# Performance work log

Hardware: AMD Instinct MI355X
Metric: run time of the kernel (lower is better)

The kernel has to match this reference:

```python
import jax, jax.numpy as jnp
import numpy as np

B, DIM, H, W = 8, 256, 128, 128
P = 4               # patch_size
HEADS = 8
HD = DIM // HEADS   # head dim = 32
CPB_HIDDEN = 512    # hidden width of the dynamic RPE MLP


def setup_inputs() -> dict:
    key = jax.random.key(0)
    ks = jax.random.split(key, 12)
    s = 0.02
    return {
        "x": jax.random.normal(ks[0], (B, DIM, H, W), dtype=jnp.float32),
        # PatchEmbed2d: Conv2d(dim, dim, kernel=P, stride=P)  weight [O, I, P, P]
        "w_embed": jax.random.normal(ks[1], (DIM, DIM, P, P), dtype=jnp.float32) * s,
        "b_embed": jnp.zeros((DIM,), dtype=jnp.float32),
        # DynamicPosEncoder: MLP(2 -> CPB_HIDDEN -> HEADS) on relative coords
        "cpb_w1": jax.random.normal(ks[2], (CPB_HIDDEN, 2), dtype=jnp.float32) * s,
        "cpb_b1": jnp.zeros((CPB_HIDDEN,), dtype=jnp.float32),
        "cpb_w2": jax.random.normal(ks[3], (HEADS, CPB_HIDDEN), dtype=jnp.float32) * s,
        # MaskAttention2d
        "w_qkv": jax.random.normal(ks[4], (3 * DIM, DIM), dtype=jnp.float32) * s,
        "b_qkv": jnp.zeros((3 * DIM,), dtype=jnp.float32),
        "w_proj": jax.random.normal(ks[5], (DIM, DIM), dtype=jnp.float32) * s,
        "b_proj": jnp.zeros((DIM,), dtype=jnp.float32),
        # PatchUnEmbed2d: ConvTranspose2d(dim, dim, kernel=P, stride=P)  weight [I, O, P, P]
        "w_unembed": jax.random.normal(ks[6], (DIM, DIM, P, P), dtype=jnp.float32) * s,
        "b_unembed": jnp.zeros((DIM,), dtype=jnp.float32),
    }


def _rpe_bias(Hp, Wp, cpb_w1, cpb_b1, cpb_w2):
    """Dynamic relative position bias -> [HEADS, N, N], N = Hp*Wp."""
    # continuous relative-coordinate table [(2Hp-1)*(2Wp-1), 2], normalized to [-1, 1]
    rh = (jnp.arange(2 * Hp - 1, dtype=jnp.float32) - (Hp - 1)) / max(Hp - 1, 1)
    rw = (jnp.arange(2 * Wp - 1, dtype=jnp.float32) - (Wp - 1)) / max(Wp - 1, 1)
    rel = jnp.stack(jnp.meshgrid(rh, rw, indexing="ij"), axis=-1).reshape(-1, 2)
    table = jax.nn.relu(rel @ cpb_w1.T + cpb_b1) @ cpb_w2.T  # [(2Hp-1)(2Wp-1), HEADS]
    # static relative position index [N, N]
    ch = np.arange(Hp)
    cw = np.arange(Wp)
    coords = np.stack(np.meshgrid(ch, cw, indexing="ij")).reshape(2, -1)  # [2, N]
    d = coords[:, :, None] - coords[:, None, :]                           # [2, N, N]
    idx = (d[0] + Hp - 1) * (2 * Wp - 1) + (d[1] + Wp - 1)               # [N, N]
    bias = table[jnp.asarray(idx)]                                        # [N, N, HEADS]
    return bias.transpose(2, 0, 1)                                        # [HEADS, N, N]


def reference(x, w_embed, b_embed, cpb_w1, cpb_b1, cpb_w2,
              w_qkv, b_qkv, w_proj, b_proj, w_unembed, b_unembed):
    Bx, C, Hf, Wf = x.shape
    Hp, Wp = Hf // P, Wf // P
    N = Hp * Wp
    # ---- patch embed: Conv2d(k=P, s=P) as block reshape + einsum ----
    xr = x.reshape(Bx, C, Hp, P, Wp, P)
    z = jnp.einsum("bchpwq,ocpq->bohw", xr, w_embed) + b_embed[None, :, None, None]
    # ---- dynamic RPE bias ----
    bias = _rpe_bias(Hp, Wp, cpb_w1, cpb_b1, cpb_w2)  # [HEADS, N, N]
    # ---- multi-head self-attention over the Hp*Wp grid ----
    tok = z.reshape(Bx, C, N).transpose(0, 2, 1)                     # [B, N, C]
    qkv = tok @ w_qkv.T + b_qkv                                       # [B, N, 3C]
    qkv = qkv.reshape(Bx, N, 3, HEADS, HD).transpose(2, 0, 3, 1, 4)   # [3, B, H, N, hd]
    q, k, v = qkv[0], qkv[1], qkv[2]
    scale = HD ** -0.5
    attn = jnp.einsum("bhnd,bhmd->bhnm", q * scale, k) + bias[None]   # [B, H, N, N]
    attn = jax.nn.softmax(attn, axis=-1)
    out = jnp.einsum("bhnm,bhmd->bhnd", attn, v)                      # [B, H, N, hd]
    out = out.transpose(0, 2, 1, 3).reshape(Bx, N, C)
    out = out @ w_proj.T + b_proj                                     # [B, N, C]
    z2 = out.transpose(0, 2, 1).reshape(Bx, C, Hp, Wp)
    # ---- patch unembed: ConvTranspose2d(k=P, s=P) as einsum + block reshape ----
    y = jnp.einsum("bchw,copq->bohpwq", z2, w_unembed)
    y = y.reshape(Bx, C, Hf, Wf) + b_unembed[None, :, None, None]
    return y
```

## Files before the change

### kernel.cpp

```cpp
#include <hip/hip_runtime.h>
#include <cstdint>
#include <cstddef>


typedef __bf16 bf16x8 __attribute__((ext_vector_type(8)));
typedef float f32x4 __attribute__((ext_vector_type(4)));
typedef unsigned short u16x4 __attribute__((ext_vector_type(4)));

__device__ __forceinline__ unsigned short f2bf(float f) {
  unsigned u = __builtin_bit_cast(unsigned, f);
  u += 0x7fffu + ((u >> 16) & 1u);
  return (unsigned short)(u >> 16);
}
__device__ __forceinline__ float bf2f(unsigned short u) {
  return __builtin_bit_cast(float, ((unsigned)u) << 16);
}

__device__ __forceinline__ void async_ld16(const void* g, void* l) {
  __builtin_amdgcn_global_load_lds(
      (const __attribute__((address_space(1))) void*)g,
      (__attribute__((address_space(3))) void*)l, 16, 0, 0);
}

__global__ __launch_bounds__(256) void rpe_table_kernel(
    const float* __restrict__ w1, const float* __restrict__ b1,
    const float* __restrict__ w2, float* __restrict__ tableT) {
  int t = blockIdx.x * 256 + threadIdx.x;
  if (t >= 3969) return;
  int a = t / 63, c = t - a * 63;
  float rh = (float)(a - 31) * (1.0f / 31.0f);
  float rw = (float)(c - 31) * (1.0f / 31.0f);
  float acc[8];
#pragma unroll
  for (int h = 0; h < 8; h++) acc[h] = 0.f;
  for (int j = 0; j < 512; j++) {
    float hv = fmaxf(rh * w1[2 * j] + rw * w1[2 * j + 1] + b1[j], 0.f);
#pragma unroll
    for (int h = 0; h < 8; h++) acc[h] += hv * w2[h * 512 + j];
  }
#pragma unroll
  for (int h = 0; h < 8; h++) tableT[h * 4096 + t] = acc[h];
}

__global__ __launch_bounds__(256) void cvt_bf16_kernel(
    const float* __restrict__ src, unsigned short* __restrict__ dst, int n8) {
  int i = blockIdx.x * 256 + threadIdx.x;
  if (i >= n8) return;
  const float4* s4 = (const float4*)src + (size_t)i * 2;
  float4 a = s4[0], b = s4[1];
  unsigned short t[8] = {f2bf(a.x), f2bf(a.y), f2bf(a.z), f2bf(a.w),
                         f2bf(b.x), f2bf(b.y), f2bf(b.z), f2bf(b.w)};
  *(uint4*)(dst + (size_t)i * 8) = *(const uint4*)t;
}

__global__ __launch_bounds__(256) void transpose_cvt_kernel(
    const float* __restrict__ src, unsigned short* __restrict__ dst) {
  __shared__ float tile[32][33];
  int bx = blockIdx.x;
  int by = blockIdx.y;
  int tx = threadIdx.x & 31, ty = threadIdx.x >> 5;
#pragma unroll
  for (int r = 0; r < 32; r += 8)
    tile[ty + r][tx] = src[(size_t)(by * 32 + ty + r) * 4096 + bx * 32 + tx];
  __syncthreads();
#pragma unroll
  for (int r = 0; r < 32; r += 8)
    dst[(size_t)(bx * 32 + ty + r) * 256 + by * 32 + tx] = f2bf(tile[tx][ty + r]);
}

__global__ __launch_bounds__(256) void im2col_bf16_kernel(
    const float* __restrict__ x, unsigned short* __restrict__ A) {
  int gid = blockIdx.x * 256 + threadIdx.x;
  int bn = gid & 8191;
  int c = gid >> 13;
  int b = bn >> 10;
  int hw = bn & 1023;
  int h = hw >> 5, w = hw & 31;
  const float4* x4 = (const float4*)x;
  int base = ((b * 256 + c) * 128 + 4 * h) * 32 + w;
  unsigned short t[16];
#pragma unroll
  for (int p = 0; p < 4; p++) {
    float4 v = x4[base + p * 32];
    t[p * 4 + 0] = f2bf(v.x); t[p * 4 + 1] = f2bf(v.y);
    t[p * 4 + 2] = f2bf(v.z); t[p * 4 + 3] = f2bf(v.w);
  }
  unsigned short* dst = A + (size_t)bn * 4096 + c * 16;
  *(uint4*)dst = *(const uint4*)t;
  *(uint4*)(dst + 8) = *(const uint4*)(t + 8);
}

__global__ __launch_bounds__(256) void splitk_reduce_kernel(
    const float* __restrict__ part, const float* __restrict__ bias,
    unsigned short* __restrict__ out) {
  size_t i = ((size_t)blockIdx.x * 256 + threadIdx.x) * 8;
  const float4* p = (const float4*)(part + i);
  const size_t s4 = 2097152 / 4;
  float4 a0 = p[0], a1 = p[1];
#pragma unroll
  for (int s = 1; s < 4; s++) {
    float4 b0 = p[s * s4], b1 = p[s * s4 + 1];
    a0.x += b0.x; a0.y += b0.y; a0.z += b0.z; a0.w += b0.w;
    a1.x += b1.x; a1.y += b1.y; a1.z += b1.z; a1.w += b1.w;
  }
  int col = (int)(i & 255);
  unsigned short t8[8] = {
      f2bf(a0.x + bias[col + 0]), f2bf(a0.y + bias[col + 1]),
      f2bf(a0.z + bias[col + 2]), f2bf(a0.w + bias[col + 3]),
      f2bf(a1.x + bias[col + 4]), f2bf(a1.y + bias[col + 5]),
      f2bf(a1.z + bias[col + 6]), f2bf(a1.w + bias[col + 7])};
  *(uint4*)(out + i) = *(const uint4*)t8;
}

template <int CMODE>
__global__ __launch_bounds__(256) void gemm_mfma_kernel(
    const unsigned short* __restrict__ A, const unsigned short* __restrict__ B,
    const float* __restrict__ bias, void* __restrict__ Cv,
    int M, int N, int K, int lda, int ldb, int ldc) {
  __shared__ unsigned short As[2 * 128 * 32];
  __shared__ unsigned short Bs[2 * 128 * 32];
  int tid = threadIdx.x;
  int lane = tid & 63;
  int wave = tid >> 6;
  int m0 = blockIdx.y * 128, n0 = blockIdx.x * 128;
  int wm = (wave & 1) * 64, wn = (wave >> 1) * 64;

  if (CMODE == 4) {
    int s = blockIdx.z;
    A += (size_t)s * K;
    B += (size_t)s * K;
    Cv = (void*)((float*)Cv + (size_t)s * M * N);
  }

  f32x4 acc[4][4];
#pragma unroll
  for (int i = 0; i < 4; i++)
#pragma unroll
    for (int j = 0; j < 4; j++) acc[i][j] = (f32x4){0.f, 0.f, 0.f, 0.f};

  int f0 = tid, f1 = tid + 256;
  const unsigned short* Ag0 = A + (size_t)(m0 + (f0 >> 2)) * lda + (f0 & 3) * 8;
  const unsigned short* Ag1 = A + (size_t)(m0 + (f1 >> 2)) * lda + (f1 & 3) * 8;
  const unsigned short* Bg0 = B + (size_t)(n0 + (f0 >> 2)) * ldb + (f0 & 3) * 8;
  const unsigned short* Bg1 = B + (size_t)(n0 + (f1 >> 2)) * ldb + (f1 & 3) * 8;
  unsigned short* Al0 = As + f0 * 8;
  unsigned short* Al1 = As + f1 * 8;
  unsigned short* Bl0 = Bs + f0 * 8;
  unsigned short* Bl1 = Bs + f1 * 8;

  int fr = lane & 15;
  int fh = lane >> 4;

  int ntiles = K >> 5;
  async_ld16(Ag0, Al0);
  async_ld16(Ag1, Al1);
  async_ld16(Bg0, Bl0);
  async_ld16(Bg1, Bl1);
  __syncthreads();

  for (int t = 0; t < ntiles; t++) {
    int cur = (t & 1) << 12;
    int nxt = cur ^ 4096;
    if (t + 1 < ntiles) {
      int kn = (t + 1) << 5;
      async_ld16(Ag0 + kn, Al0 + nxt);
      async_ld16(Ag1 + kn, Al1 + nxt);
      async_ld16(Bg0 + kn, Bl0 + nxt);
      async_ld16(Bg1 + kn, Bl1 + nxt);
    }
    const unsigned short* Asc = As + cur;
    const unsigned short* Bsc = Bs + cur;
    bf16x8 af[4], bfr[4];
#pragma unroll
    for (int tt = 0; tt < 4; tt++) {
      af[tt] = *(const bf16x8*)(Asc + (wm + tt * 16 + fr) * 32 + fh * 8);
      bfr[tt] = *(const bf16x8*)(Bsc + (wn + tt * 16 + fr) * 32 + fh * 8);
    }
#pragma unroll
    for (int mt = 0; mt < 4; mt++)
#pragma unroll
      for (int nt = 0; nt < 4; nt++)
        acc[mt][nt] = __builtin_amdgcn_mfma_f32_16x16x32_bf16(
            af[mt], bfr[nt], acc[mt][nt], 0, 0, 0);
    __syncthreads();
  }

#pragma unroll
  for (int mt = 0; mt < 4; mt++) {
    int row0 = m0 + wm + mt * 16 + fh * 4;
    if (CMODE == 2) {
      int b = row0 >> 10, hp = (row0 >> 5) & 31, wp = row0 & 31;
      size_t rowoff0 = (size_t)b * 4194304 + hp * 512 + wp * 4;
      float* y = (float*)Cv;
#pragma unroll
      for (int nt = 0; nt < 4; nt++) {
        int col = n0 + wn + nt * 16 + fr;
        int o = col >> 4, p = (col >> 2) & 3, q = col & 3;
        size_t coloff = (size_t)o * 16384 + p * 128 + q;
        float bv = bias[o];
#pragma unroll
        for (int r = 0; r < 4; r++)
          y[rowoff0 + r * 4 + coloff] = acc[mt][nt][r] + bv;
      }
    } else if (CMODE == 3) {
      unsigned short* base = (unsigned short*)Cv;
#pragma unroll
      for (int nt = 0; nt < 4; nt++) {
        int col = n0 + wn + nt * 16 + fr;
        int which = col >> 8, hh = (col >> 5) & 7, d = col & 31;
        float bv = bias[col];
#pragma unroll
        for (int r = 0; r < 4; r++) {
          int row = row0 + r;
          int bb = row >> 10, nn = row & 1023;
          int bh = bb * 8 + hh;
          float v = acc[mt][nt][r] + bv;
          if (which == 0) v *= 0.17677669529663687f;
          size_t addr;
          if (which < 2)
            addr = (size_t)which * 2097152 + ((size_t)bh * 1024 + nn) * 32 + d;
          else
            addr = (size_t)2 * 2097152 + (size_t)bh * 32768 + (size_t)d * 1024 + nn;
          base[addr] = f2bf(v);
        }
      }
    } else if (CMODE == 4) {
      float* Cp = (float*)Cv;
#pragma unroll
      for (int nt = 0; nt < 4; nt++) {
        int col = n0 + wn + nt * 16 + fr;
#pragma unroll
        for (int r = 0; r < 4; r++)
          Cp[(size_t)(row0 + r) * ldc + col] = acc[mt][nt][r];
      }
    } else {
#pragma unroll
      for (int nt = 0; nt < 4; nt++) {
        int col = n0 + wn + nt * 16 + fr;
        float bv = bias ? bias[col] : 0.f;
        unsigned short* C = (unsigned short*)Cv;
#pragma unroll
        for (int r = 0; r < 4; r++)
          C[(size_t)(row0 + r) * ldc + col] = f2bf(acc[mt][nt][r] + bv);
      }
    }
  }
}

__global__ __launch_bounds__(512) void attn_mfma_kernel(
    const unsigned short* __restrict__ Qb, const unsigned short* __restrict__ Kb,
    const unsigned short* __restrict__ Vtb,
    const float* __restrict__ tableT,
    unsigned short* __restrict__ out) {
  __shared__ float smf[12804];
  float* th = smf;
  unsigned short* Ks = (unsigned short*)(smf + 3972);
  unsigned short* Vt = (unsigned short*)(smf + 6276);
  unsigned short* Ps = (unsigned short*)(smf + 8452);
  unsigned short* Qs = (unsigned short*)(smf + 8452);

  int tid = threadIdx.x;
  int lane = tid & 63, w = tid >> 6;
  int n = lane & 15, g = lane >> 4;
  int blk = blockIdx.x;
  int qt = blk & 7, b = (blk >> 3) & 7, h = blk >> 6;
  int bh = b * 8 + h;
  int q0 = qt * 128;

  const unsigned short* Qg = Qb + ((size_t)bh * 1024 + q0) * 32;
  const unsigned short* Kg = Kb + (size_t)bh * 1024 * 32;
  const unsigned short* Vg = Vtb + (size_t)bh * 32 * 1024;
  const float* tg = tableT + (size_t)h * 4096;

  {
    int r = tid >> 2, c = tid & 3;
    *(uint4*)(Qs + r * 36 + c * 8) = *(const uint4*)(Qg + (size_t)r * 32 + c * 8);
  }
  for (int i = tid; i < 3969; i += 512) th[i] = tg[i];

  bool isK = tid < 256;
  int cidx = isK ? tid : tid - 256;
  const unsigned short* gsrc = isK
      ? (Kg + (size_t)(cidx >> 2) * 32 + (cidx & 3) * 8)
      : (Vg + (size_t)(cidx >> 3) * 1024 + (cidx & 7) * 8);
  int gstep = isK ? 2048 : 64;
  unsigned short* lbase = isK ? Ks : Vt;
  int loff = isK ? ((cidx >> 2) * 36 + (cidx & 3) * 8)
                 : ((cidx >> 3) * 68 + (cidx & 7) * 8);
  int lbufstep = isK ? 2304 : 2176;

  uint4 greg = *(const uint4*)(gsrc);
  __syncthreads();

  bf16x8 qf = *(const bf16x8*)(Qs + (w * 16 + n) * 36 + g * 8);

  *(uint4*)(lbase + loff) = greg;
  greg = *(const uint4*)(gsrc + gstep);
  __syncthreads();

  f32x4 oacc[2];
#pragma unroll
  for (int i = 0; i < 2; i++) oacc[i] = (f32x4){0.f, 0.f, 0.f, 0.f};
  float m_run = -1e30f, l_run = 0.f;

  unsigned short* Pw = Ps + w * 1088;
  int q = q0 + w * 16 + n;
  int qh = q >> 5, qw = q & 31;

  for (int t = 0; t < 16; t++) {
    const unsigned short* Kc = Ks + (t & 1) * 2304;
    const unsigned short* Vc = Vt + (t & 1) * 2176;
    int k0 = t * 64;

    f32x4 s[4];
    __builtin_amdgcn_s_setprio(1);
#pragma unroll
    for (int mt = 0; mt < 4; mt++) {
      bf16x8 kf = *(const bf16x8*)(Kc + (mt * 16 + n) * 36 + g * 8);
      s[mt] = __builtin_amdgcn_mfma_f32_16x16x32_bf16(
          kf, qf, (f32x4){0.f, 0.f, 0.f, 0.f}, 0, 0, 0);
    }
    __builtin_amdgcn_s_setprio(0);

#pragma unroll
    for (int mt = 0; mt < 4; mt++) {
      int kb = k0 + mt * 16 + g * 4;
      int ib = (qh - (kb >> 5) + 31) * 63 + (qw - (kb & 31) + 31);
      s[mt][0] += th[ib];
      s[mt][1] += th[ib - 1];
      s[mt][2] += th[ib - 2];
      s[mt][3] += th[ib - 3];
    }

    float mx = -1e30f;
#pragma unroll
    for (int mt = 0; mt < 4; mt++)
#pragma unroll
      for (int r = 0; r < 4; r++) mx = fmaxf(mx, s[mt][r]);
    mx = fmaxf(mx, __shfl_xor(mx, 16, 64));
    mx = fmaxf(mx, __shfl_xor(mx, 32, 64));
    float m_new = fmaxf(m_run, mx);
    float alpha = __expf(m_run - m_new);
    m_run = m_new;
    float ls = 0.f;
#pragma unroll
    for (int mt = 0; mt < 4; mt++) {
#pragma unroll
      for (int r = 0; r < 4; r++) {
        float p = __expf(s[mt][r] - m_new);
        s[mt][r] = p;
        ls += p;
      }
      u16x4 pk = {f2bf(s[mt][0]), f2bf(s[mt][1]), f2bf(s[mt][2]),
                  f2bf(s[mt][3])};
      *(u16x4*)(Pw + n * 68 + mt * 16 + g * 4) = pk;
    }
    ls += __shfl_xor(ls, 16, 64);
    ls += __shfl_xor(ls, 32, 64);
    l_run = l_run * alpha + ls;

#pragma unroll
    for (int dt = 0; dt < 2; dt++)
#pragma unroll
      for (int r = 0; r < 4; r++) oacc[dt][r] *= alpha;
    __builtin_amdgcn_s_setprio(1);
#pragma unroll
    for (int kt = 0; kt < 2; kt++) {
      bf16x8 vf0 = *(const bf16x8*)(Vc + n * 68 + kt * 32 + g * 8);
      bf16x8 vf1 = *(const bf16x8*)(Vc + (16 + n) * 68 + kt * 32 + g * 8);
      bf16x8 pf = *(const bf16x8*)(Pw + n * 68 + kt * 32 + g * 8);
      oacc[0] = __builtin_amdgcn_mfma_f32_16x16x32_bf16(vf0, pf, oacc[0], 0, 0, 0);
      oacc[1] = __builtin_amdgcn_mfma_f32_16x16x32_bf16(vf1, pf, oacc[1], 0, 0, 0);
    }
    __builtin_amdgcn_s_setprio(0);

    if (t < 15) {
      *(uint4*)(lbase + ((t + 1) & 1) * lbufstep + loff) = greg;
      if (t < 14) greg = *(const uint4*)(gsrc + (size_t)(t + 2) * gstep);
    }
    __syncthreads();
  }

  float invl = 1.f / l_run;
  unsigned short* ob = out + ((size_t)(b * 1024 + q) * 256) + h * 32;
#pragma unroll
  for (int dt = 0; dt < 2; dt++) {
    u16x4 o4 = {f2bf(oacc[dt][0] * invl), f2bf(oacc[dt][1] * invl),
                f2bf(oacc[dt][2] * invl), f2bf(oacc[dt][3] * invl)};
    *(u16x4*)(ob + dt * 16 + g * 4) = o4;
  }
}

extern "C" void kernel_launch(void* const* d_in, const int* in_sizes, int n_in,
                              void* d_out, int out_size, void* d_ws, size_t ws_size,
                              hipStream_t stream) {
  const float* x         = (const float*)d_in[0];
  const float* w_embed   = (const float*)d_in[1];
  const float* b_embed   = (const float*)d_in[2];
  const float* cpb_w1    = (const float*)d_in[3];
  const float* cpb_b1    = (const float*)d_in[4];
  const float* cpb_w2    = (const float*)d_in[5];
  const float* w_qkv     = (const float*)d_in[6];
  const float* b_qkv     = (const float*)d_in[7];
  const float* w_proj    = (const float*)d_in[8];
  const float* b_proj    = (const float*)d_in[9];
  const float* w_unembed = (const float*)d_in[10];
  const float* b_unembed = (const float*)d_in[11];
  float* out = (float*)d_out;

  char* w = (char*)d_ws;
  unsigned short* Abig  = (unsigned short*)w; w += (size_t)8192 * 4096 * 2;
  unsigned short* tok   = (unsigned short*)w; w += (size_t)8192 * 256 * 2;
  unsigned short* wE    = (unsigned short*)w; w += (size_t)1048576 * 2;
  unsigned short* wQ    = (unsigned short*)w; w += (size_t)196608 * 2;
  unsigned short* wP    = (unsigned short*)w; w += (size_t)65536 * 2;
  unsigned short* wUt   = (unsigned short*)w; w += (size_t)1048576 * 2;
  float*          tableT= (float*)w;          w += (size_t)32768 * 4;
  float*          PART  = (float*)w;          w += (size_t)8388608 * 4;

  unsigned short* qkvB  = (unsigned short*)PART;
  unsigned short* attno = (unsigned short*)((char*)PART + 12582912);
  unsigned short* z2    = (unsigned short*)((char*)PART + 16777216);
  unsigned short* Qb  = qkvB;
  unsigned short* Kb  = qkvB + 2097152;
  unsigned short* Vtb = qkvB + 2 * 2097152;

  cvt_bf16_kernel<<<512, 256, 0, stream>>>(w_embed, wE, 131072);
  cvt_bf16_kernel<<<96, 256, 0, stream>>>(w_qkv, wQ, 24576);
  cvt_bf16_kernel<<<32, 256, 0, stream>>>(w_proj, wP, 8192);
  transpose_cvt_kernel<<<dim3(128, 8), 256, 0, stream>>>(w_unembed, wUt);
  im2col_bf16_kernel<<<8192, 256, 0, stream>>>(x, Abig);
  rpe_table_kernel<<<16, 256, 0, stream>>>(cpb_w1, cpb_b1, cpb_w2, tableT);

  gemm_mfma_kernel<4><<<dim3(2, 64, 4), 256, 0, stream>>>(
      Abig, wE, nullptr, PART, 8192, 256, 1024, 4096, 4096, 256);
  splitk_reduce_kernel<<<1024, 256, 0, stream>>>(PART, b_embed, tok);

  gemm_mfma_kernel<3><<<dim3(6, 64), 256, 0, stream>>>(
      tok, wQ, b_qkv, qkvB, 8192, 768, 256, 256, 256, 0);

  attn_mfma_kernel<<<512, 512, 0, stream>>>(Qb, Kb, Vtb, tableT, attno);

  gemm_mfma_kernel<4><<<dim3(2, 64, 4), 256, 0, stream>>>(
      attno, wP, nullptr, (float*)Abig, 8192, 256, 64, 256, 256, 256);
  splitk_reduce_kernel<<<1024, 256, 0, stream>>>((float*)Abig, b_proj, z2);

  gemm_mfma_kernel<2><<<dim3(32, 64), 256, 0, stream>>>(
      z2, wUt, b_unembed, out, 8192, 4096, 256, 256, 256, 0);
}
```

Before: 562.4 us.

## Load K/V fragments directly from global into registers, drop LDS staging and barriers

The attention kernel no longer stages K and V tiles through shared memory with a block-wide barrier each iteration. Each wave now reads its MFMA fragments straight from global memory, prefetching the next K tile into registers and double-buffering the per-wave P tile in LDS. The row-sum reduction across lanes moves out of the loop to the end, the block index order changes so that neighbouring blocks share a query tile across heads, and the loop is fully unrolled. In exchange, every wave re-reads K/V from global or L2, raising memory traffic and register pressure.

```diff
diff --git a/kernel.cpp b/kernel.cpp
--- a/kernel.cpp
+++ b/kernel.cpp
@@ -252,18 +252,14 @@
     const unsigned short* __restrict__ Vtb,
     const float* __restrict__ tableT,
     unsigned short* __restrict__ out) {
-  __shared__ float smf[12804];
-  float* th = smf;
-  unsigned short* Ks = (unsigned short*)(smf + 3972);
-  unsigned short* Vt = (unsigned short*)(smf + 6276);
-  unsigned short* Ps = (unsigned short*)(smf + 8452);
-  unsigned short* Qs = (unsigned short*)(smf + 8452);
+  __shared__ float th[3972];
+  __shared__ unsigned short Ps[2][8][1088];
 
   int tid = threadIdx.x;
   int lane = tid & 63, w = tid >> 6;
   int n = lane & 15, g = lane >> 4;
   int blk = blockIdx.x;
-  int qt = blk & 7, b = (blk >> 3) & 7, h = blk >> 6;
+  int h = blk & 7, b = (blk >> 3) & 7, qt = blk >> 6;
   int bh = b * 8 + h;
   int q0 = qt * 128;
 
@@ -272,60 +268,56 @@
   const unsigned short* Vg = Vtb + (size_t)bh * 32 * 1024;
   const float* tg = tableT + (size_t)h * 4096;
 
-  {
-    int r = tid >> 2, c = tid & 3;
-    *(uint4*)(Qs + r * 36 + c * 8) = *(const uint4*)(Qg + (size_t)r * 32 + c * 8);
-  }
   for (int i = tid; i < 3969; i += 512) th[i] = tg[i];
 
-  bool isK = tid < 256;
-  int cidx = isK ? tid : tid - 256;
-  const unsigned short* gsrc = isK
-      ? (Kg + (size_t)(cidx >> 2) * 32 + (cidx & 3) * 8)
-      : (Vg + (size_t)(cidx >> 3) * 1024 + (cidx & 7) * 8);
-  int gstep = isK ? 2048 : 64;
-  unsigned short* lbase = isK ? Ks : Vt;
-  int loff = isK ? ((cidx >> 2) * 36 + (cidx & 3) * 8)
-                 : ((cidx >> 3) * 68 + (cidx & 7) * 8);
-  int lbufstep = isK ? 2304 : 2176;
-
-  uint4 greg = *(const uint4*)(gsrc);
+  bf16x8 qf = *(const bf16x8*)(Qg + (size_t)(w * 16 + n) * 32 + g * 8);
+
   __syncthreads();
 
-  bf16x8 qf = *(const bf16x8*)(Qs + (w * 16 + n) * 36 + g * 8);
-
-  *(uint4*)(lbase + loff) = greg;
-  greg = *(const uint4*)(gsrc + gstep);
-  __syncthreads();
-
   f32x4 oacc[2];
-#pragma unroll
-  for (int i = 0; i < 2; i++) oacc[i] = (f32x4){0.f, 0.f, 0.f, 0.f};
+  oacc[0] = (f32x4){0.f, 0.f, 0.f, 0.f};
+  oacc[1] = (f32x4){0.f, 0.f, 0.f, 0.f};
   float m_run = -1e30f, l_run = 0.f;
 
-  unsigned short* Pw = Ps + w * 1088;
   int q = q0 + w * 16 + n;
-  int qh = q >> 5, qw = q & 31;
-
+  int tbase = (q >> 5) * 63 + (q & 31);
+
+  unsigned short* Pw0 = &Ps[0][w][0];
+  unsigned short* Pw1 = &Ps[1][w][0];
+
+  bf16x8 kf[2][4], vf[4];
+#pragma unroll
+  for (int mt = 0; mt < 4; mt++)
+    kf[0][mt] = *(const bf16x8*)(Kg + (size_t)(mt * 16 + n) * 32 + g * 8);
+
+#pragma unroll
   for (int t = 0; t < 16; t++) {
-    const unsigned short* Kc = Ks + (t & 1) * 2304;
-    const unsigned short* Vc = Vt + (t & 1) * 2176;
-    int k0 = t * 64;
+    const int cur = t & 1, nxt = cur ^ 1;
+    const int k0 = t * 64;
+
+#pragma unroll
+    for (int i = 0; i < 4; i++)
+      vf[i] = *(const bf16x8*)(Vg + (size_t)((i & 1) * 16 + n) * 1024 + k0 +
+                               (i >> 1) * 32 + g * 8);
+    if (t < 15) {
+#pragma unroll
+      for (int mt = 0; mt < 4; mt++)
+        kf[nxt][mt] = *(const bf16x8*)(Kg + (size_t)(k0 + 64 + mt * 16 + n) * 32 +
+                                       g * 8);
+    }
 
     f32x4 s[4];
     __builtin_amdgcn_s_setprio(1);
 #pragma unroll
-    for (int mt = 0; mt < 4; mt++) {
-      bf16x8 kf = *(const bf16x8*)(Kc + (mt * 16 + n) * 36 + g * 8);
+    for (int mt = 0; mt < 4; mt++)
       s[mt] = __builtin_amdgcn_mfma_f32_16x16x32_bf16(
-          kf, qf, (f32x4){0.f, 0.f, 0.f, 0.f}, 0, 0, 0);
-    }
+          kf[cur][mt], qf, (f32x4){0.f, 0.f, 0.f, 0.f}, 0, 0, 0);
     __builtin_amdgcn_s_setprio(0);
 
 #pragma unroll
     for (int mt = 0; mt < 4; mt++) {
       int kb = k0 + mt * 16 + g * 4;
-      int ib = (qh - (kb >> 5) + 31) * 63 + (qw - (kb & 31) + 31);
+      int ib = tbase + (31 - (kb >> 5)) * 63 + (31 - (kb & 31));
       s[mt][0] += th[ib];
       s[mt][1] += th[ib - 1];
       s[mt][2] += th[ib - 2];
@@ -342,6 +334,8 @@
     float m_new = fmaxf(m_run, mx);
     float alpha = __expf(m_run - m_new);
     m_run = m_new;
+
+    unsigned short* Pw = cur ? Pw1 : Pw0;
     float ls = 0.f;
 #pragma unroll
     for (int mt = 0; mt < 4; mt++) {
@@ -355,8 +349,6 @@
                   f2bf(s[mt][3])};
       *(u16x4*)(Pw + n * 68 + mt * 16 + g * 4) = pk;
     }
-    ls += __shfl_xor(ls, 16, 64);
-    ls += __shfl_xor(ls, 32, 64);
     l_run = l_run * alpha + ls;
 
 #pragma unroll
@@ -366,22 +358,19 @@
     __builtin_amdgcn_s_setprio(1);
 #pragma unroll
     for (int kt = 0; kt < 2; kt++) {
-      bf16x8 vf0 = *(const bf16x8*)(Vc + n * 68 + kt * 32 + g * 8);
-      bf16x8 vf1 = *(const bf16x8*)(Vc + (16 + n) * 68 + kt * 32 + g * 8);
       bf16x8 pf = *(const bf16x8*)(Pw + n * 68 + kt * 32 + g * 8);
-      oacc[0] = __builtin_amdgcn_mfma_f32_16x16x32_bf16(vf0, pf, oacc[0], 0, 0, 0);
-      oacc[1] = __builtin_amdgcn_mfma_f32_16x16x32_bf16(vf1, pf, oacc[1], 0, 0, 0);
+      oacc[0] = __builtin_amdgcn_mfma_f32_16x16x32_bf16(vf[kt * 2 + 0], pf,
+                                                        oacc[0], 0, 0, 0);
+      oacc[1] = __builtin_amdgcn_mfma_f32_16x16x32_bf16(vf[kt * 2 + 1], pf,
+                                                        oacc[1], 0, 0, 0);
     }
     __builtin_amdgcn_s_setprio(0);
-
-    if (t < 15) {
-      *(uint4*)(lbase + ((t + 1) & 1) * lbufstep + loff) = greg;
-      if (t < 14) greg = *(const uint4*)(gsrc + (size_t)(t + 2) * gstep);
-    }
-    __syncthreads();
-  }
-
-  float invl = 1.f / l_run;
+  }
+
+  float l = l_run;
+  l += __shfl_xor(l, 16, 64);
+  l += __shfl_xor(l, 32, 64);
+  float invl = 1.f / l;
   unsigned short* ob = out + ((size_t)(b * 1024 + q) * 256) + h * 32;
 #pragma unroll
   for (int dt = 0; dt < 2; dt++) {
```

Result: faster. 547.4 us (-2.7%).
